# Performance work log

Hardware: AMD Instinct MI355X
Metric: run time of the kernel (lower is better)

Reference implementation:

```python
import jax, jax.numpy as jnp
import numpy as np

T = 512           # num_timestamps
D = 512           # video_embed_dim
V = 2048          # fmri_dim (voxels)
H = 128           # hidden_dim


def setup_inputs() -> dict:
    key = jax.random.key(0)
    k = jax.random.split(key, 8)
    s1 = 1.0 / np.sqrt(D)
    s2 = 1.0 / np.sqrt(H)
    return {
        "video_embeddings": jax.random.normal(k[0], (T, D), dtype=jnp.float32),
        # stacked per-voxel weights (torch Linear: y = x @ W.T + b; we store W already transposed as [in, out])
        "W1": jax.random.uniform(k[1], (V, D, H), jnp.float32, -s1, s1),
        "b1": jax.random.uniform(k[2], (V, H), jnp.float32, -s1, s1),
        "W2": jax.random.uniform(k[3], (V, H, H), jnp.float32, -s2, s2),
        "b2": jax.random.uniform(k[4], (V, H), jnp.float32, -s2, s2),
        "W3": jax.random.uniform(k[5], (V, H), jnp.float32, -s2, s2),
        "b3": jax.random.uniform(k[6], (V,), jnp.float32, -s2, s2),
    }


def reference(video_embeddings, W1, b1, W2, b2, W3, b3):
    # Per-voxel MLP expressed as batched GEMMs over the voxel axis.
    # Dropout is identity in eval mode.
    h = jax.nn.relu(jnp.einsum("td,vdh->tvh", video_embeddings, W1) + b1)  # [T,V,H]
    h = jax.nn.relu(jnp.einsum("tvh,vhg->tvg", h, W2) + b2)                 # [T,V,H]
    out = jnp.einsum("tvh,vh->tv", h, W3) + b3                               # [T,V]
    return out
```

## Files before the change

### kernel.cpp

```cpp
#include <hip/hip_runtime.h>
#include <hip/hip_bf16.h>

#define TT 512
#define DD 512
#define VV 2048
#define HH 128

typedef __attribute__((ext_vector_type(8))) short bf16x8;
typedef __attribute__((ext_vector_type(8))) unsigned short ushort8;
typedef __attribute__((ext_vector_type(4))) unsigned short ushort4v;
typedef __attribute__((ext_vector_type(4))) float f32x4;

__device__ __forceinline__ unsigned short f2bf(float f) {
  union { __hip_bfloat16 b; unsigned short u; } cv;
  cv.b = __float2bfloat16(f);
  return cv.u;
}

__device__ __forceinline__ void lds_barrier() {
  asm volatile("s_waitcnt lgkmcnt(0)\n\ts_barrier" ::: "memory");
}

__global__ void cvt_x_kernel(const float* __restrict__ x, unsigned short* __restrict__ xb) {
  const int i = blockIdx.x * blockDim.x + threadIdx.x;
  const float4 f = ((const float4*)x)[i];
  ushort4v u;
  u[0] = f2bf(f.x); u[1] = f2bf(f.y); u[2] = f2bf(f.z); u[3] = f2bf(f.w);
  ((ushort4v*)xb)[i] = u;
}

__global__ __launch_bounds__(512, 2)
void voxel_mlp_kernel(const unsigned short* __restrict__ Xb,
                      const float* __restrict__ W1,
                      const float* __restrict__ b1,
                      const float* __restrict__ W2,
                      const float* __restrict__ b2,
                      const float* __restrict__ W3,
                      const float* __restrict__ b3,
                      float* __restrict__ out) {
  __shared__ __align__(16) char LDS[65536];
  constexpr unsigned W2BASE = 0;
  constexpr unsigned R1     = 32768;
  constexpr unsigned H1BASE = 32768;

  const int v   = blockIdx.x;
  const int tid = threadIdx.x;
  const int w   = tid >> 6;
  const int l   = tid & 63;
  const int lg  = l >> 4;
  const int ll  = l & 15;

  const float* W1v = W1 + (size_t)v * DD * HH;
  const float* W2v = W2 + (size_t)v * HH * HH;

  const int      cn    = (l >> 3) & 7;
  const unsigned xorv  = (unsigned)(cn & 7) << 4;
  const unsigned wsl1  = (unsigned)(w >> 2) * 8192u + (unsigned)cn * 1024u;
  const unsigned woff1 = ((unsigned)((w & 3) * 256 + (l & 7) * 32)) ^ xorv;
  const unsigned wsl2  = (unsigned)cn * 1024u;
  const unsigned woff2 = ((unsigned)((w >> 1) * 256 + (l & 7) * 32 + (w & 1) * 8)) ^ xorv;

  float2 w1s[2][8];
  float2 w2s[2][4];

#define ISSUE_W1(t)                                                        \
  { const float* gp = W1v + ((t) * 64 + w * 8) * HH + 2 * l;               \
    _Pragma("unroll") for (int j = 0; j < 8; ++j)                          \
      w1s[(t) & 1][j] = *(const float2*)(gp + j * HH); }

#define CVT_W1(t)                                                          \
  { ushort8 e0, e1;                                                        \
    _Pragma("unroll") for (int j = 0; j < 8; ++j) {                        \
      e0[j] = f2bf(w1s[(t) & 1][j].x);                                     \
      e1[j] = f2bf(w1s[(t) & 1][j].y); }                                   \
    const unsigned b_ = R1 + (unsigned)((t) & 1) * 16384u + wsl1;          \
    *(ushort8*)(&LDS[b_ + woff1]) = e0;                                    \
    *(ushort8*)(&LDS[b_ + (woff1 ^ 16u)]) = e1; }

#define ISSUE_W2(s)                                                        \
  { const float* gp = W2v + ((s) * 32 + w * 4) * HH + 2 * l;               \
    _Pragma("unroll") for (int j = 0; j < 4; ++j)                          \
      w2s[(s) & 1][j] = *(const float2*)(gp + j * HH); }

#define CVT_W2(s)                                                          \
  { ushort4v e0, e1;                                                       \
    _Pragma("unroll") for (int j = 0; j < 4; ++j) {                        \
      e0[j] = f2bf(w2s[(s) & 1][j].x);                                     \
      e1[j] = f2bf(w2s[(s) & 1][j].y); }                                   \
    const unsigned b_ = W2BASE + (unsigned)(s) * 8192u + wsl2;             \
    *(ushort4v*)(&LDS[b_ + woff2]) = e0;                                   \
    *(ushort4v*)(&LDS[b_ + (woff2 ^ 16u)]) = e1; }

  ISSUE_W1(0);
  ISSUE_W1(1);
  CVT_W1(0);
  lds_barrier();

  f32x4 acc1[4][8];
#pragma unroll
  for (int mi = 0; mi < 4; ++mi)
#pragma unroll
    for (int n = 0; n < 8; ++n) acc1[mi][n] = f32x4{0.f, 0.f, 0.f, 0.f};

#pragma unroll
  for (int s = 0; s < 8; ++s) {
    bf16x8 aS[2][4];
#pragma unroll
    for (int u = 0; u < 2; ++u)
#pragma unroll
      for (int mi = 0; mi < 4; ++mi)
        aS[u][mi] = *(const bf16x8*)(Xb + (size_t)(w * 64 + mi * 16 + ll) * DD +
                                     s * 64 + u * 32 + lg * 8);

    if (s + 2 < 8) ISSUE_W1(s + 2);
    if (s < 4)     ISSUE_W2(s);

#pragma unroll
    for (int u = 0; u < 2; ++u)
#pragma unroll
      for (int n = 0; n < 8; ++n) {
        const bf16x8 b = *(const bf16x8*)(&LDS[R1 + (unsigned)(s & 1) * 16384u +
                                               (unsigned)u * 8192u + (unsigned)n * 1024u +
                                               (((unsigned)l * 16u) ^ ((unsigned)(n & 7) << 4))]);
#pragma unroll
        for (int mi = 0; mi < 4; ++mi)
          acc1[mi][n] = __builtin_amdgcn_mfma_f32_16x16x32_bf16(aS[u][mi], b, acc1[mi][n], 0, 0, 0);
      }

    if (s < 7)            CVT_W1(s + 1);
    if (s >= 1 && s <= 4) CVT_W2(s - 1);
    lds_barrier();
  }

#undef ISSUE_W1
#undef ISSUE_W2
#undef CVT_W1
#undef CVT_W2

  float b1v[8], b2v[8], w3v[8];
#pragma unroll
  for (int n = 0; n < 8; ++n) {
    b1v[n] = b1[v * HH + n * 16 + ll];
    b2v[n] = b2[v * HH + n * 16 + ll];
    w3v[n] = W3[v * HH + n * 16 + ll];
  }
  const float b3v = b3[v];

  const unsigned slot = H1BASE + (unsigned)w * 4096u;

#pragma unroll
  for (int mi = 0; mi < 4; ++mi) {
#pragma unroll
    for (int n = 0; n < 8; ++n) {
#pragma unroll
      for (int r = 0; r < 4; ++r) {
        const int tl = lg * 4 + r;
        float hv = acc1[mi][n][r] + b1v[n];
        hv = fmaxf(hv, 0.f);
        const int h = n * 16 + ll;
        const unsigned byte = slot + (unsigned)tl * 256u +
                              (unsigned)((h * 2) ^ ((tl & 7) << 4));
        *(unsigned short*)(&LDS[byte]) = f2bf(hv);
      }
    }
    f32x4 acc2[8];
#pragma unroll
    for (int m = 0; m < 8; ++m) acc2[m] = f32x4{0.f, 0.f, 0.f, 0.f};
#pragma unroll
    for (int ki = 0; ki < 4; ++ki) {
      const int k0 = ki * 32 + lg * 8;
      const unsigned abyte = slot + (unsigned)ll * 256u +
                             (unsigned)((k0 * 2) ^ ((ll & 7) << 4));
      const bf16x8 a2 = *(const bf16x8*)(&LDS[abyte]);
#pragma unroll
      for (int m = 0; m < 8; ++m) {
        const bf16x8 bw = *(const bf16x8*)(&LDS[W2BASE + (unsigned)ki * 8192u +
                                                (unsigned)m * 1024u +
                                                (((unsigned)l * 16u) ^ ((unsigned)(m & 7) << 4))]);
        acc2[m] = __builtin_amdgcn_mfma_f32_16x16x32_bf16(a2, bw, acc2[m], 0, 0, 0);
      }
    }
#pragma unroll
    for (int r = 0; r < 4; ++r) {
      float p = 0.f;
#pragma unroll
      for (int m = 0; m < 8; ++m)
        p += fmaxf(acc2[m][r] + b2v[m], 0.f) * w3v[m];
      p += __shfl_xor(p, 1);
      p += __shfl_xor(p, 2);
      p += __shfl_xor(p, 4);
      p += __shfl_xor(p, 8);
      if (ll == 0) {
        const int t = w * 64 + mi * 16 + lg * 4 + r;
        out[t * VV + v] = p + b3v;
      }
    }
  }
}

extern "C" void kernel_launch(void* const* d_in, const int* in_sizes, int n_in,
                              void* d_out, int out_size, void* d_ws, size_t ws_size,
                              hipStream_t stream) {
  const float* X  = (const float*)d_in[0];
  const float* W1 = (const float*)d_in[1];
  const float* b1 = (const float*)d_in[2];
  const float* W2 = (const float*)d_in[3];
  const float* b2 = (const float*)d_in[4];
  const float* W3 = (const float*)d_in[5];
  const float* b3 = (const float*)d_in[6];
  float* out = (float*)d_out;

  unsigned short* Xb = (unsigned short*)d_ws;

  cvt_x_kernel<<<256, 256, 0, stream>>>(X, Xb);
  voxel_mlp_kernel<<<VV, 512, 0, stream>>>(Xb, W1, b1, W2, b2, W3, b3, out);
}
```

Baseline: 305.6 us.

## Load bf16 high halves of fp32 weights directly via a unified 3-stage pipeline

Replaces the fp32 float2 loads and round-to-nearest bf16 conversion of W1 and W2 with 16-bit loads of the upper half of each fp32 word, which truncates to bf16 and removes the conversion ALU work. W1 and W2 staging are merged into one 10-step, 3-deep register pipeline. The LDS write for the next step now happens before the MFMA loop rather than after it. The trade-offs are twice as many narrower global load instructions, unchanged DRAM traffic since whole cache lines are still fetched, and slightly different numerics from truncation instead of rounding.

```diff
diff --git a/kernel.cpp b/kernel.cpp
--- a/kernel.cpp
+++ b/kernel.cpp
@@ -50,50 +50,37 @@
   const int lg  = l >> 4;
   const int ll  = l & 15;
 
-  const float* W1v = W1 + (size_t)v * DD * HH;
-  const float* W2v = W2 + (size_t)v * HH * HH;
-
-  const int      cn    = (l >> 3) & 7;
-  const unsigned xorv  = (unsigned)(cn & 7) << 4;
-  const unsigned wsl1  = (unsigned)(w >> 2) * 8192u + (unsigned)cn * 1024u;
-  const unsigned woff1 = ((unsigned)((w & 3) * 256 + (l & 7) * 32)) ^ xorv;
-  const unsigned wsl2  = (unsigned)cn * 1024u;
-  const unsigned woff2 = ((unsigned)((w >> 1) * 256 + (l & 7) * 32 + (w & 1) * 8)) ^ xorv;
-
-  float2 w1s[2][8];
-  float2 w2s[2][4];
-
-#define ISSUE_W1(t)                                                        \
-  { const float* gp = W1v + ((t) * 64 + w * 8) * HH + 2 * l;               \
-    _Pragma("unroll") for (int j = 0; j < 8; ++j)                          \
-      w1s[(t) & 1][j] = *(const float2*)(gp + j * HH); }
-
-#define CVT_W1(t)                                                          \
-  { ushort8 e0, e1;                                                        \
-    _Pragma("unroll") for (int j = 0; j < 8; ++j) {                        \
-      e0[j] = f2bf(w1s[(t) & 1][j].x);                                     \
-      e1[j] = f2bf(w1s[(t) & 1][j].y); }                                   \
-    const unsigned b_ = R1 + (unsigned)((t) & 1) * 16384u + wsl1;          \
-    *(ushort8*)(&LDS[b_ + woff1]) = e0;                                    \
-    *(ushort8*)(&LDS[b_ + (woff1 ^ 16u)]) = e1; }
-
-#define ISSUE_W2(s)                                                        \
-  { const float* gp = W2v + ((s) * 32 + w * 4) * HH + 2 * l;               \
-    _Pragma("unroll") for (int j = 0; j < 4; ++j)                          \
-      w2s[(s) & 1][j] = *(const float2*)(gp + j * HH); }
-
-#define CVT_W2(s)                                                          \
-  { ushort4v e0, e1;                                                       \
-    _Pragma("unroll") for (int j = 0; j < 4; ++j) {                        \
-      e0[j] = f2bf(w2s[(s) & 1][j].x);                                     \
-      e1[j] = f2bf(w2s[(s) & 1][j].y); }                                   \
-    const unsigned b_ = W2BASE + (unsigned)(s) * 8192u + wsl2;             \
-    *(ushort4v*)(&LDS[b_ + woff2]) = e0;                                   \
-    *(ushort4v*)(&LDS[b_ + (woff2 ^ 16u)]) = e1; }
-
-  ISSUE_W1(0);
-  ISSUE_W1(1);
-  CVT_W1(0);
+  const unsigned short* W1us = (const unsigned short*)(W1 + (size_t)v * DD * HH);
+  const unsigned short* W2us = (const unsigned short*)(W2 + (size_t)v * HH * HH);
+
+  unsigned stg[3][16];
+
+#define ISSUE_STG(t)                                                        \
+  { const unsigned short* gp =                                              \
+      ((t) < 8 ? W1us + (t) * 64 * 2 * HH : W2us + ((t) - 8) * 64 * 2 * HH) \
+      + (w * 8) * 2 * HH + 1;                                               \
+    _Pragma("unroll") for (int jr = 0; jr < 8; ++jr) {                      \
+      stg[(t) % 3][jr]     = gp[jr * 2 * HH + 2 * l];                       \
+      stg[(t) % 3][8 + jr] = gp[jr * 2 * HH + 2 * (64 + l)]; } }
+
+#define CVT_STG(t)                                                          \
+  { ushort8 e0, e1;                                                         \
+    _Pragma("unroll") for (int jr = 0; jr < 8; ++jr) {                      \
+      e0[jr] = (unsigned short)stg[(t) % 3][jr];                            \
+      e1[jr] = (unsigned short)stg[(t) % 3][8 + jr]; }                      \
+    const unsigned base_ =                                                  \
+      ((t) < 8 ? R1 + (unsigned)((t) & 1) * 16384u                          \
+               : W2BASE + (unsigned)((t) - 8) * 16384u)                     \
+      + (unsigned)(w >> 2) * 8192u;                                         \
+    const unsigned wb = (unsigned)((w & 3) * 256 + (l & 15) * 16);          \
+    const unsigned n0 = (unsigned)(l >> 4), n1 = n0 + 4u;                   \
+    *(ushort8*)(&LDS[base_ + n0 * 1024u + (wb ^ (n0 << 4))]) = e0;          \
+    *(ushort8*)(&LDS[base_ + n1 * 1024u + (wb ^ (n1 << 4))]) = e1; }
+
+  ISSUE_STG(0);
+  ISSUE_STG(1);
+  ISSUE_STG(2);
+  CVT_STG(0);
   lds_barrier();
 
   f32x4 acc1[4][8];
@@ -112,8 +99,9 @@
         aS[u][mi] = *(const bf16x8*)(Xb + (size_t)(w * 64 + mi * 16 + ll) * DD +
                                      s * 64 + u * 32 + lg * 8);
 
-    if (s + 2 < 8) ISSUE_W1(s + 2);
-    if (s < 4)     ISSUE_W2(s);
+    if (s + 3 <= 9) ISSUE_STG(s + 3);
+
+    CVT_STG(s + 1);
 
 #pragma unroll
     for (int u = 0; u < 2; ++u)
@@ -127,15 +115,14 @@
           acc1[mi][n] = __builtin_amdgcn_mfma_f32_16x16x32_bf16(aS[u][mi], b, acc1[mi][n], 0, 0, 0);
       }
 
-    if (s < 7)            CVT_W1(s + 1);
-    if (s >= 1 && s <= 4) CVT_W2(s - 1);
     lds_barrier();
   }
 
-#undef ISSUE_W1
-#undef ISSUE_W2
-#undef CVT_W1
-#undef CVT_W2
+  CVT_STG(9);
+  lds_barrier();
+
+#undef ISSUE_STG
+#undef CVT_STG
 
   float b1v[8], b2v[8], w3v[8];
 #pragma unroll
```

Result: slower. 578.9 us (+89.4%).
